# Kernel tuning notes

Measured on AMD Instinct MI355X. Metric: run time of the kernel, lower is better.

The kernel has to match this reference:

```python
import jax, jax.numpy as jnp
import numpy as np

N = 200000      # nodes
E = 200000      # edges per direction
IN = 256        # in_dim
HID = 256       # hidden_dim
HEADS = 4
C = HID // HEADS  # 64 per-head channels
OUT = 128
EPS = 1e-5      # LayerNorm eps (torch default)


def _ln(x, g, b):
    m = jnp.mean(x, axis=-1, keepdims=True)
    v = jnp.mean(jnp.square(x - m), axis=-1, keepdims=True)
    return (x - m) / jnp.sqrt(v + EPS) * g + b


def _gat(x, W, att_src, att_dst, bias, edge_index):
    """PyG GATConv (default args: add_self_loops=True, negative_slope=0.2, concat heads)."""
    n = x.shape[0]
    loops = jnp.arange(n, dtype=edge_index.dtype)
    ei = jnp.concatenate([edge_index, jnp.stack([loops, loops])], axis=1)
    src, dst = ei[0], ei[1]
    h = (x @ W).reshape(n, HEADS, C)                      # [N,H,C]
    a_src = jnp.sum(h * att_src, axis=-1)                 # [N,H]
    a_dst = jnp.sum(h * att_dst, axis=-1)                 # [N,H]
    e = jax.nn.leaky_relu(a_src[src] + a_dst[dst], 0.2)   # [E+N,H]
    m = jax.ops.segment_max(e, dst, num_segments=n)       # per-dst softmax max
    ex = jnp.exp(e - m[dst])
    denom = jax.ops.segment_sum(ex, dst, num_segments=n)
    alpha = ex / denom[dst]                               # [E+N,H]
    out = jax.ops.segment_sum(h[src] * alpha[..., None], dst, num_segments=n)
    return out.reshape(n, HEADS * C) + bias


def setup_inputs() -> dict:
    key = jax.random.key(0)
    ks = jax.random.split(key, 20)
    w = lambda k, s, sc=0.05: jax.random.normal(k, s, jnp.float32) * sc
    return {
        "x": jax.random.normal(ks[0], (N, IN), jnp.float32),
        "edge_index_bu": jax.random.randint(ks[1], (2, E), 0, N, jnp.int32),
        "edge_index_td": jax.random.randint(ks[2], (2, E), 0, N, jnp.int32),
        "Wp": w(ks[3], (IN, HID)), "bp": jnp.zeros((HID,), jnp.float32),
        "W_bu": w(ks[4], (HID, HID)), "asrc_bu": w(ks[5], (HEADS, C)),
        "adst_bu": w(ks[6], (HEADS, C)), "bias_bu": jnp.zeros((HID,), jnp.float32),
        "W_td": w(ks[7], (HID, HID)), "asrc_td": w(ks[8], (HEADS, C)),
        "adst_td": w(ks[9], (HEADS, C)), "bias_td": jnp.zeros((HID,), jnp.float32),
        "Wf": w(ks[10], (2 * HID, OUT)), "bf": jnp.zeros((OUT,), jnp.float32),
        "g_bu": jnp.ones((HID,), jnp.float32), "b_bu": jnp.zeros((HID,), jnp.float32),
        "g_td": jnp.ones((HID,), jnp.float32), "b_td": jnp.zeros((HID,), jnp.float32),
        "g_out": jnp.ones((OUT,), jnp.float32), "b_out": jnp.zeros((OUT,), jnp.float32),
    }


def reference(x, edge_index_bu, edge_index_td, Wp, bp,
              W_bu, asrc_bu, adst_bu, bias_bu,
              W_td, asrc_td, adst_td, bias_td,
              Wf, bf, g_bu, b_bu, g_td, b_td, g_out, b_out):
    h = jax.nn.relu(x @ Wp + bp)  # dropout is identity in eval
    x_bu = jax.nn.relu(_ln(_gat(h, W_bu, asrc_bu, adst_bu, bias_bu, edge_index_bu), g_bu, b_bu))
    x_td = jax.nn.relu(_ln(_gat(h, W_td, asrc_td, adst_td, bias_td, edge_index_td), g_td, b_td))
    out = jnp.concatenate([x_bu, x_td], axis=-1) @ Wf + bf
    out = _ln(out, g_out, b_out)
    nrm = jnp.sqrt(jnp.sum(jnp.square(out), axis=-1, keepdims=True))
    return out / jnp.maximum(nrm, 1e-12)
```

## Files before the change

### kernel.cpp

```cpp
#include <hip/hip_runtime.h>
#include <hip/hip_bf16.h>
#include <stdint.h>


typedef __attribute__((ext_vector_type(8))) short bf16x8;
typedef __attribute__((ext_vector_type(4))) short bf16x4;
typedef __attribute__((ext_vector_type(4))) float f32x4;

#define HID 256

__device__ __forceinline__ float red16(float v) {
    #pragma unroll
    for (int o = 1; o < 16; o <<= 1) v += __shfl_xor(v, o, 64);
    return v;
}
__device__ __forceinline__ float bf2f(short s) {
    return __uint_as_float(((unsigned)(unsigned short)s) << 16);
}

__device__ __forceinline__ void gload_lds16(const void* g, void* l) {
    __builtin_amdgcn_global_load_lds(
        reinterpret_cast<const __attribute__((address_space(1))) uint32_t*>(
            reinterpret_cast<uintptr_t>(g)),
        reinterpret_cast<__attribute__((address_space(3))) uint32_t*>(
            reinterpret_cast<uintptr_t>(l)),
        16, 0, 0);
}

__global__ __launch_bounds__(256) void transpose_all(
    const float* __restrict__ Wp, const float* __restrict__ Wbu,
    const float* __restrict__ Wtd, const float* __restrict__ Wf,
    __hip_bfloat16* __restrict__ Wpt, __hip_bfloat16* __restrict__ Wcat,
    __hip_bfloat16* __restrict__ Wft) {
    int idx = blockIdx.x * 256 + threadIdx.x;
    if (idx < 65536) {
        int k = idx >> 8, j = idx & 255;
        Wpt[j * 256 + k] = __float2bfloat16(Wp[idx]);
    } else if (idx < 131072) {
        int t = idx - 65536; int k = t >> 8, j = t & 255;
        Wcat[j * 256 + k] = __float2bfloat16(Wbu[t]);
    } else if (idx < 196608) {
        int t = idx - 131072; int k = t >> 8, j = t & 255;
        Wcat[65536 + j * 256 + k] = __float2bfloat16(Wtd[t]);
    } else if (idx < 262144) {
        int t = idx - 196608; int k = t >> 7, j = t & 127;
        Wft[(long)j * 512 + k] = __float2bfloat16(Wf[t]);
    }
}

template<int BN, int MODE, int CVT>
__global__ __launch_bounds__(512) void gemm_tiled(
    const float* __restrict__ Af, const __hip_bfloat16* __restrict__ Ab, int lda,
    const __hip_bfloat16* __restrict__ Bt, int KI,
    const float* __restrict__ bias, int doRelu,
    __hip_bfloat16* __restrict__ outB, int ldcB, int colOff,
    float* __restrict__ outF,
    const float* __restrict__ gw, const float* __restrict__ bw, int N) {

    constexpr int WN = BN / 64;
    constexpr int WM = 8 / WN;
    constexpr int MR = (128 / WM) / 16;

    __shared__ __align__(16) __hip_bfloat16 sA[2][128 * 32];
    __shared__ __align__(16) __hip_bfloat16 sB[2][BN * 32];
    __shared__ float sRed[MODE == 2 ? 128 * 4 : 4];
    __shared__ float sN2[MODE == 2 ? 128 * 2 : 2];

    int tid = threadIdx.x;
    int wv = tid >> 6, ln = tid & 63;
    int m = ln & 15, q = ln >> 4;
    long row0 = (long)blockIdx.x * 128;
    int wr = (wv / WN) * (128 / WM);
    int wc = (wv % WN) * 64;

    f32x4 acc[MR][4];
    #pragma unroll
    for (int mi = 0; mi < MR; ++mi)
        #pragma unroll
        for (int t = 0; t < 4; ++t) acc[mi][t] = (f32x4){0.f, 0.f, 0.f, 0.f};

    int oA = tid * 16;
    long rowA = row0 + (oA >> 6);
    if (rowA >= N) rowA = N - 1;
    int kel = (oA & 63) >> 1;
    long aBase = rowA * (long)lda + kel;

    auto stage = [&](int buf, int k0) {
        if constexpr (CVT) {
            const float* src = Af + aBase + k0;
            f32x4 fa0 = *(const f32x4*)src;
            f32x4 fa1 = *(const f32x4*)(src + 4);
            __hip_bfloat16 t8[8];
            t8[0] = __float2bfloat16(fa0[0]); t8[1] = __float2bfloat16(fa0[1]);
            t8[2] = __float2bfloat16(fa0[2]); t8[3] = __float2bfloat16(fa0[3]);
            t8[4] = __float2bfloat16(fa1[0]); t8[5] = __float2bfloat16(fa1[1]);
            t8[6] = __float2bfloat16(fa1[2]); t8[7] = __float2bfloat16(fa1[3]);
            *(bf16x8*)((char*)sA[buf] + oA) = *(const bf16x8*)t8;
        } else {
            gload_lds16(Ab + aBase + k0, (char*)sA[buf] + oA);
        }
        #pragma unroll
        for (int j = 0; j < BN / 128; ++j) {
            int o = j * 8192 + tid * 16;
            const __hip_bfloat16* src = Bt + (long)(o >> 6) * KI + k0 + ((o & 63) >> 1);
            gload_lds16(src, (char*)sB[buf] + o);
        }
    };

    auto compute = [&](int buf) {
        bf16x8 af[MR], bfr[4];
        #pragma unroll
        for (int mi = 0; mi < MR; ++mi)
            af[mi] = *(const bf16x8*)((const char*)sA[buf] + ((wr + mi * 16 + m) << 6) + q * 16);
        #pragma unroll
        for (int t = 0; t < 4; ++t)
            bfr[t] = *(const bf16x8*)((const char*)sB[buf] + ((wc + t * 16 + m) << 6) + q * 16);
        #pragma unroll
        for (int mi = 0; mi < MR; ++mi)
            #pragma unroll
            for (int t = 0; t < 4; ++t)
                acc[mi][t] = __builtin_amdgcn_mfma_f32_16x16x32_bf16(af[mi], bfr[t],
                                                                     acc[mi][t], 0, 0, 0);
    };

    stage(0, 0);
    __syncthreads();
    int cur = 0;
    for (int k0 = 0; k0 < KI; k0 += 32) {
        if (k0 + 32 < KI) stage(cur ^ 1, k0 + 32);
        compute(cur);
        __syncthreads();
        cur ^= 1;
    }

    if constexpr (MODE != 2) {
        #pragma unroll
        for (int mi = 0; mi < MR; ++mi) {
            #pragma unroll
            for (int t = 0; t < 4; ++t) {
                int col = wc + t * 16 + m;
                float bv = bias ? bias[col] : 0.f;
                #pragma unroll
                for (int r = 0; r < 4; ++r) {
                    long row = row0 + wr + mi * 16 + q * 4 + r;
                    if (row < N) {
                        float v = acc[mi][t][r] + bv;
                        if (doRelu) v = fmaxf(v, 0.f);
                        outB[row * ldcB + colOff + col] = __float2bfloat16(v);
                    }
                }
            }
        }
    }

    if constexpr (MODE == 2) {
        float vv[MR][4][4];
        float gcol[4], bcol[4];
        #pragma unroll
        for (int t = 0; t < 4; ++t) {
            int col = wc + t * 16 + m;
            float bb = bias[col];
            gcol[t] = gw[col]; bcol[t] = bw[col];
            #pragma unroll
            for (int mi = 0; mi < MR; ++mi)
                #pragma unroll
                for (int r = 0; r < 4; ++r) vv[mi][t][r] = acc[mi][t][r] + bb;
        }
        int wcid = wc >> 6;
        __syncthreads();
        #pragma unroll
        for (int mi = 0; mi < MR; ++mi) {
            #pragma unroll
            for (int r = 0; r < 4; ++r) {
                float s1 = vv[mi][0][r] + vv[mi][1][r] + vv[mi][2][r] + vv[mi][3][r];
                float s2 = vv[mi][0][r] * vv[mi][0][r] + vv[mi][1][r] * vv[mi][1][r]
                         + vv[mi][2][r] * vv[mi][2][r] + vv[mi][3][r] * vv[mi][3][r];
                s1 = red16(s1); s2 = red16(s2);
                if (m == 0) {
                    int lrow = wr + mi * 16 + q * 4 + r;
                    sRed[lrow * 4 + wcid * 2 + 0] = s1;
                    sRed[lrow * 4 + wcid * 2 + 1] = s2;
                }
            }
        }
        __syncthreads();
        #pragma unroll
        for (int mi = 0; mi < MR; ++mi) {
            #pragma unroll
            for (int r = 0; r < 4; ++r) {
                int lrow = wr + mi * 16 + q * 4 + r;
                float S1 = sRed[lrow * 4 + 0] + sRed[lrow * 4 + 2];
                float S2 = sRed[lrow * 4 + 1] + sRed[lrow * 4 + 3];
                float mean = S1 * (1.f / 128.f);
                float var = S2 * (1.f / 128.f) - mean * mean;
                float inv = rsqrtf(fmaxf(var, 0.f) + 1e-5f);
                float n2 = 0.f;
                #pragma unroll
                for (int t = 0; t < 4; ++t) {
                    float y = (vv[mi][t][r] - mean) * inv * gcol[t] + bcol[t];
                    vv[mi][t][r] = y;
                    n2 += y * y;
                }
                n2 = red16(n2);
                if (m == 0) sN2[lrow * 2 + wcid] = n2;
            }
        }
        __syncthreads();
        #pragma unroll
        for (int mi = 0; mi < MR; ++mi) {
            #pragma unroll
            for (int r = 0; r < 4; ++r) {
                int lrow = wr + mi * 16 + q * 4 + r;
                long row = row0 + lrow;
                float nrm = sqrtf(sN2[lrow * 2] + sN2[lrow * 2 + 1]);
                float sc = 1.f / fmaxf(nrm, 1e-12f);
                if (row < N) {
                    #pragma unroll
                    for (int t = 0; t < 4; ++t)
                        outF[row * 128 + wc + t * 16 + m] = vv[mi][t][r] * sc;
                }
            }
        }
    }
}

__global__ __launch_bounds__(1024) void gemm_dir2(
    const __hip_bfloat16* __restrict__ Ab,
    const __hip_bfloat16* __restrict__ Bt,
    const float* __restrict__ asrc0, const float* __restrict__ adst0,
    const float* __restrict__ asrc1, const float* __restrict__ adst1,
    float* __restrict__ aS0, float* __restrict__ aD0,
    float* __restrict__ aS1, float* __restrict__ aD1,
    __hip_bfloat16* __restrict__ outB, int N) {
    constexpr int KI = 256;
    __shared__ __align__(16) __hip_bfloat16 sA[2][128 * 32];
    __shared__ __align__(16) __hip_bfloat16 sB[2][512 * 32];

    int tid = threadIdx.x;
    int wv = tid >> 6, ln = tid & 63;
    int m = ln & 15, q = ln >> 4;
    long row0 = (long)blockIdx.x * 128;
    int wr = (wv >> 3) * 64;
    int wc = (wv & 7) * 64;

    f32x4 acc[4][4];
    #pragma unroll
    for (int mi = 0; mi < 4; ++mi)
        #pragma unroll
        for (int t = 0; t < 4; ++t) acc[mi][t] = (f32x4){0.f, 0.f, 0.f, 0.f};

    int oA = (tid & 511) * 16;
    long rowA = row0 + (oA >> 6);
    if (rowA >= N) rowA = N - 1;
    int kel = (oA & 63) >> 1;
    long aBase = rowA * (long)KI + kel;
    int oB0 = tid * 16;

    auto stage = [&](int buf, int k0) {
        if (tid < 512) gload_lds16(Ab + aBase + k0, (char*)sA[buf] + oA);
        #pragma unroll
        for (int j = 0; j < 2; ++j) {
            int o = j * 16384 + oB0;
            const __hip_bfloat16* src = Bt + (long)(o >> 6) * KI + k0 + ((o & 63) >> 1);
            gload_lds16(src, (char*)sB[buf] + o);
        }
    };
    auto compute = [&](int buf) {
        bf16x8 af[4], bfr[4];
        #pragma unroll
        for (int mi = 0; mi < 4; ++mi)
            af[mi] = *(const bf16x8*)((const char*)sA[buf] + ((wr + mi * 16 + m) << 6) + q * 16);
        #pragma unroll
        for (int t = 0; t < 4; ++t)
            bfr[t] = *(const bf16x8*)((const char*)sB[buf] + ((wc + t * 16 + m) << 6) + q * 16);
        #pragma unroll
        for (int mi = 0; mi < 4; ++mi)
            #pragma unroll
            for (int t = 0; t < 4; ++t)
                acc[mi][t] = __builtin_amdgcn_mfma_f32_16x16x32_bf16(af[mi], bfr[t],
                                                                     acc[mi][t], 0, 0, 0);
    };

    stage(0, 0);
    __syncthreads();
    int cur = 0;
    for (int k0 = 0; k0 < KI; k0 += 32) {
        if (k0 + 32 < KI) stage(cur ^ 1, k0 + 32);
        compute(cur);
        __syncthreads();
        cur ^= 1;
    }

    #pragma unroll
    for (int mi = 0; mi < 4; ++mi) {
        #pragma unroll
        for (int t = 0; t < 4; ++t) {
            int col = wc + t * 16 + m;
            #pragma unroll
            for (int r = 0; r < 4; ++r) {
                long row = row0 + wr + mi * 16 + q * 4 + r;
                if (row < N) outB[row * 512 + col] = __float2bfloat16(acc[mi][t][r]);
            }
        }
    }

    int dir = wc >> 8;
    int cc = wc & 255;
    int h = cc >> 6;
    const float* as_ = dir ? asrc1 : asrc0;
    const float* ad_ = dir ? adst1 : adst0;
    float* aS = dir ? aS1 : aS0;
    float* aD = dir ? aD1 : aD0;
    f32x4 sw, dw;
    #pragma unroll
    for (int t = 0; t < 4; ++t) {
        sw[t] = as_[cc + t * 16 + m];
        dw[t] = ad_[cc + t * 16 + m];
    }
    #pragma unroll
    for (int mi = 0; mi < 4; ++mi) {
        #pragma unroll
        for (int r = 0; r < 4; ++r) {
            float ps = acc[mi][0][r] * sw[0] + acc[mi][1][r] * sw[1]
                     + acc[mi][2][r] * sw[2] + acc[mi][3][r] * sw[3];
            float pd = acc[mi][0][r] * dw[0] + acc[mi][1][r] * dw[1]
                     + acc[mi][2][r] * dw[2] + acc[mi][3][r] * dw[3];
            ps = red16(ps); pd = red16(pd);
            long row = row0 + wr + mi * 16 + q * 4 + r;
            if (m == 0 && row < N) {
                aS[row * 4 + h] = ps;
                aD[row * 4 + h] = pd;
            }
        }
    }
}

__global__ __launch_bounds__(256) void hist_dst2(const int* __restrict__ ei0,
                                                 const int* __restrict__ ei1,
                                                 int E, int N, int* __restrict__ cnt) {
    int e = blockIdx.x * 256 + threadIdx.x;
    if (e < E) atomicAdd(&cnt[ei0[E + e]], 1);
    else if (e < 2 * E) atomicAdd(&cnt[ei1[e] + N], 1);
}

__global__ __launch_bounds__(256) void scan1(const int* __restrict__ cnt,
                                             int* __restrict__ offpart,
                                             int* __restrict__ bsum, int n) {
    int t = threadIdx.x, i = blockIdx.x * 256 + t;
    int lane = t & 63, w = t >> 6;
    int v = (i < n) ? cnt[i] : 0;
    int inc = v;
    #pragma unroll
    for (int o = 1; o < 64; o <<= 1) {
        int u = __shfl_up(inc, o, 64);
        if (lane >= o) inc += u;
    }
    __shared__ int wsum[4];
    if (lane == 63) wsum[w] = inc;
    __syncthreads();
    int wadd = 0;
    #pragma unroll
    for (int k = 0; k < 4; ++k) if (k < w) wadd += wsum[k];
    if (i < n) offpart[i] = inc - v + wadd;
    if (t == 255) bsum[blockIdx.x] = inc + wadd;
}

__global__ __launch_bounds__(256) void scan2(const int* __restrict__ bsum,
                                             int* __restrict__ btot, int nb) {
    int t = threadIdx.x, lane = t & 63, w = t >> 6;
    int loc[8]; int s = 0;
    #pragma unroll
    for (int k = 0; k < 8; ++k) {
        int idx = t * 8 + k;
        int v = (idx < nb) ? bsum[idx] : 0;
        loc[k] = s; s += v;
    }
    int inc = s;
    #pragma unroll
    for (int o = 1; o < 64; o <<= 1) {
        int u = __shfl_up(inc, o, 64);
        if (lane >= o) inc += u;
    }
    __shared__ int wsum[4];
    if (lane == 63) wsum[w] = inc;
    __syncthreads();
    int wadd = 0;
    #pragma unroll
    for (int k = 0; k < 4; ++k) if (k < w) wadd += wsum[k];
    int excl = inc - s + wadd;
    #pragma unroll
    for (int k = 0; k < 8; ++k) {
        int idx = t * 8 + k;
        if (idx < nb) btot[idx] = excl + loc[k];
    }
}

__global__ __launch_bounds__(256) void finalize_off(const int* __restrict__ offpart,
                                                    const int* __restrict__ btot,
                                                    int* __restrict__ off, int n, int Etot) {
    int i = blockIdx.x * 256 + threadIdx.x;
    if (i < n) off[i] = offpart[i] + btot[i >> 8];
    if (i == 0) off[n] = Etot;
}

__global__ __launch_bounds__(256) void scatter_src2(const int* __restrict__ ei0,
                                                    const int* __restrict__ ei1,
                                                    int E, int N,
                                                    const int* __restrict__ off,
                                                    int* __restrict__ cur,
                                                    int* __restrict__ esrc) {
    int e = blockIdx.x * 256 + threadIdx.x;
    if (e >= 2 * E) return;
    int d, s;
    if (e < E) { d = ei0[E + e]; s = ei0[e]; }
    else       { d = ei1[e] + N; s = ei1[e - E] + N; }
    int pos = off[d] + atomicAdd(&cur[d], 1);
    esrc[pos] = s;
}

__global__ __launch_bounds__(256) void att_alpha(
    const int* __restrict__ off, const int* __restrict__ esrc,
    const float* __restrict__ a_s, const float* __restrict__ a_d,
    float* __restrict__ alpha_self, float* __restrict__ alpha_e, int N2) {
    int d = blockIdx.x * 256 + threadIdx.x;
    if (d >= N2) return;
    int beg = off[d], end = off[d + 1];
    f32x4 adv = *(const f32x4*)(a_d + 4 * (long)d);
    f32x4 asd = *(const f32x4*)(a_s + 4 * (long)d);
    float es[4], m[4];
    #pragma unroll
    for (int h = 0; h < 4; ++h) {
        float e = asd[h] + adv[h]; e = e > 0.f ? e : 0.2f * e;
        es[h] = e; m[h] = e;
    }
    for (int j = beg; j < end; ++j) {
        int s = esrc[j];
        f32x4 asv = *(const f32x4*)(a_s + 4 * (long)s);
        #pragma unroll
        for (int h = 0; h < 4; ++h) {
            float e = asv[h] + adv[h]; e = e > 0.f ? e : 0.2f * e;
            m[h] = fmaxf(m[h], e);
        }
    }
    float sum[4];
    #pragma unroll
    for (int h = 0; h < 4; ++h) sum[h] = __expf(es[h] - m[h]);
    for (int j = beg; j < end; ++j) {
        int s = esrc[j];
        f32x4 asv = *(const f32x4*)(a_s + 4 * (long)s);
        #pragma unroll
        for (int h = 0; h < 4; ++h) {
            float e = asv[h] + adv[h]; e = e > 0.f ? e : 0.2f * e;
            sum[h] += __expf(e - m[h]);
        }
    }
    float rs[4];
    #pragma unroll
    for (int h = 0; h < 4; ++h) rs[h] = 1.f / sum[h];
    f32x4 sa;
    #pragma unroll
    for (int h = 0; h < 4; ++h) sa[h] = __expf(es[h] - m[h]) * rs[h];
    *(f32x4*)(alpha_self + 4 * (long)d) = sa;
    for (int j = beg; j < end; ++j) {
        int s = esrc[j];
        f32x4 asv = *(const f32x4*)(a_s + 4 * (long)s);
        f32x4 av;
        #pragma unroll
        for (int h = 0; h < 4; ++h) {
            float e = asv[h] + adv[h]; e = e > 0.f ? e : 0.2f * e;
            av[h] = __expf(e - m[h]) * rs[h];
        }
        *(f32x4*)(alpha_e + 4 * (long)j) = av;
    }
}

__global__ __launch_bounds__(256) void gat_gather(
    const int* __restrict__ off, const int* __restrict__ esrc,
    const float* __restrict__ alpha_self, const float* __restrict__ alpha_e,
    const __hip_bfloat16* __restrict__ hw,
    const float* __restrict__ bias0, const float* __restrict__ g0,
    const float* __restrict__ b0,
    const float* __restrict__ bias1, const float* __restrict__ g1,
    const float* __restrict__ b1,
    __hip_bfloat16* __restrict__ out, int N) {
    int tid = threadIdx.x;
    int lane = tid & 63;
    int grp = lane >> 4, li = lane & 15;
    long d = (long)blockIdx.x * 16 + (tid >> 6) * 4 + grp;
    if (d >= 2 * (long)N) return;
    int dir = d >= N;
    long dirN = (long)dir * N;
    long pd = d - dirN;
    int dirOff = dir << 8;
    const float* bias = dir ? bias1 : bias0;
    const float* g = dir ? g1 : g0;
    const float* b = dir ? b1 : b0;
    int beg = off[d], end = off[d + 1];
    int head = li >> 2;
    int c0 = li * 16;

    int j = beg;
    bool has = j < end;
    int sN = 0; float aN = 0.f;
    if (has) { sN = esrc[j]; aN = alpha_e[4 * (long)j + head]; }

    float acc[16];
    {
        float a = alpha_self[4 * d + head];
        const __hip_bfloat16* r = hw + pd * 512 + dirOff + c0;
        bf16x8 h0 = *(const bf16x8*)r;
        bf16x8 h1 = *(const bf16x8*)(r + 8);
        #pragma unroll
        for (int k = 0; k < 8; ++k) {
            acc[k] = a * bf2f(h0[k]);
            acc[8 + k] = a * bf2f(h1[k]);
        }
    }
    while (has) {
        long s = (long)sN - dirN;
        float a = aN;
        const __hip_bfloat16* r = hw + s * 512 + dirOff + c0;
        bf16x8 h0 = *(const bf16x8*)r;
        bf16x8 h1 = *(const bf16x8*)(r + 8);
        ++j; has = j < end;
        if (has) {
            sN = esrc[j];
            aN = alpha_e[4 * (long)j + head];
        }
        #pragma unroll
        for (int k = 0; k < 8; ++k) {
            acc[k] += a * bf2f(h0[k]);
            acc[8 + k] += a * bf2f(h1[k]);
        }
    }
    float s1 = 0.f, s2 = 0.f;
    #pragma unroll
    for (int k = 0; k < 16; k += 4) {
        f32x4 bi = *(const f32x4*)(bias + c0 + k);
        #pragma unroll
        for (int u = 0; u < 4; ++u) {
            float v = acc[k + u] + bi[u];
            acc[k + u] = v;
            s1 += v; s2 += v * v;
        }
    }
    #pragma unroll
    for (int o = 1; o < 16; o <<= 1) {
        s1 += __shfl_xor(s1, o, 64);
        s2 += __shfl_xor(s2, o, 64);
    }
    float mean = s1 * (1.f / 256.f);
    float var = s2 * (1.f / 256.f) - mean * mean;
    float inv = rsqrtf(fmaxf(var, 0.f) + 1e-5f);
    __hip_bfloat16 o16[16];
    #pragma unroll
    for (int k = 0; k < 16; k += 4) {
        f32x4 gv = *(const f32x4*)(g + c0 + k);
        f32x4 bv = *(const f32x4*)(b + c0 + k);
        #pragma unroll
        for (int u = 0; u < 4; ++u) {
            float y = (acc[k + u] - mean) * inv * gv[u] + bv[u];
            o16[k + u] = __float2bfloat16(fmaxf(y, 0.f));
        }
    }
    __hip_bfloat16* orow = out + pd * 512 + dirOff + c0;
    *(bf16x8*)orow = *(const bf16x8*)o16;
    *(bf16x8*)(orow + 8) = *(const bf16x8*)(o16 + 8);
}

extern "C" void kernel_launch(void* const* d_in, const int* in_sizes, int n_in,
                              void* d_out, int out_size, void* d_ws, size_t ws_size,
                              hipStream_t stream) {
    const float* x      = (const float*)d_in[0];
    const int*   ei_bu  = (const int*)d_in[1];
    const int*   ei_td  = (const int*)d_in[2];
    const float* Wp     = (const float*)d_in[3];
    const float* bp     = (const float*)d_in[4];
    const float* W_bu   = (const float*)d_in[5];
    const float* asrc_bu= (const float*)d_in[6];
    const float* adst_bu= (const float*)d_in[7];
    const float* bias_bu= (const float*)d_in[8];
    const float* W_td   = (const float*)d_in[9];
    const float* asrc_td= (const float*)d_in[10];
    const float* adst_td= (const float*)d_in[11];
    const float* bias_td= (const float*)d_in[12];
    const float* Wf     = (const float*)d_in[13];
    const float* bfv    = (const float*)d_in[14];
    const float* g_bu   = (const float*)d_in[15];
    const float* b_bu   = (const float*)d_in[16];
    const float* g_td   = (const float*)d_in[17];
    const float* b_td   = (const float*)d_in[18];
    const float* g_out  = (const float*)d_in[19];
    const float* b_out  = (const float*)d_in[20];

    const int N = in_sizes[0] / HID;
    const int E = in_sizes[1] / 2;
    const int N2 = 2 * N, E2 = 2 * E;

    char* ws = (char*)d_ws;
    size_t off0 = 0;
    auto take = [&](size_t bytes) -> char* {
        char* p = ws + off0;
        off0 += (bytes + 255) & ~(size_t)255;
        return p;
    };
    __hip_bfloat16* h_buf = (__hip_bfloat16*)take((size_t)N * 256 * 2);
    __hip_bfloat16* hwcat = (__hip_bfloat16*)take((size_t)N * 512 * 2);
    __hip_bfloat16* xcat  = (__hip_bfloat16*)take((size_t)N * 512 * 2);
    float* aS    = (float*)take((size_t)N2 * 16);
    float* aD    = (float*)take((size_t)N2 * 16);
    float* alsf  = (float*)take((size_t)N2 * 16);
    float* ale   = (float*)take((size_t)E2 * 16);
    int* cnt     = (int*)take((size_t)N2 * 4);
    int* cur     = (int*)take((size_t)N2 * 4);
    int* offpart = (int*)take((size_t)N2 * 4);
    int* offarr  = (int*)take((size_t)(N2 + 1) * 4);
    int* esrc    = (int*)take((size_t)E2 * 4);
    int* bsum    = (int*)take(2048 * 4);
    int* btot    = (int*)take(2048 * 4);
    __hip_bfloat16* Wpt  = (__hip_bfloat16*)take(256 * 256 * 2);
    __hip_bfloat16* Wcat = (__hip_bfloat16*)take(512 * 256 * 2);
    __hip_bfloat16* Wft  = (__hip_bfloat16*)take(128 * 512 * 2);

    transpose_all<<<1024, 256, 0, stream>>>(Wp, W_bu, W_td, Wf, Wpt, Wcat, Wft);

    int gm = (N + 127) / 128;

    gemm_tiled<256, 0, 1><<<gm, 512, 0, stream>>>(
        x, nullptr, 256, Wpt, 256, bp, 1, h_buf, 256, 0, nullptr,
        nullptr, nullptr, N);

    gemm_dir2<<<gm, 1024, 0, stream>>>(
        h_buf, Wcat, asrc_bu, adst_bu, asrc_td, adst_td,
        aS, aD, aS + (size_t)N * 4, aD + (size_t)N * 4, hwcat, N);

    int egrid2 = (E2 + 255) / 256;
    int ngrid2 = (N2 + 255) / 256;
    hipMemsetAsync(cnt, 0, (size_t)N2 * 8, stream);
    hist_dst2<<<egrid2, 256, 0, stream>>>(ei_bu, ei_td, E, N, cnt);
    scan1<<<ngrid2, 256, 0, stream>>>(cnt, offpart, bsum, N2);
    scan2<<<1, 256, 0, stream>>>(bsum, btot, ngrid2);
    finalize_off<<<ngrid2, 256, 0, stream>>>(offpart, btot, offarr, N2, E2);
    scatter_src2<<<egrid2, 256, 0, stream>>>(ei_bu, ei_td, E, N, offarr, cur, esrc);
    att_alpha<<<ngrid2, 256, 0, stream>>>(offarr, esrc, aS, aD, alsf, ale, N2);
    gat_gather<<<(N2 + 15) / 16, 256, 0, stream>>>(offarr, esrc, alsf, ale, hwcat,
                                                   bias_bu, g_bu, b_bu,
                                                   bias_td, g_td, b_td,
                                                   xcat, N);

    gemm_tiled<128, 2, 0><<<gm, 512, 0, stream>>>(
        nullptr, xcat, 512, Wft, 512, bfv, 0, nullptr, 128, 0, (float*)d_out,
        g_out, b_out, N);
}
```

Measured before the change: 810.8 us.

## Fuse attention softmax into gather, histogram into GEMM, zeroing into transpose

Removes the separate att_alpha kernel and computes the per-destination softmax max, sum and weights inside gat_gather per head, eliminating the alpha_self/alpha_e buffers and their writes and reads. The destination histogram is folded into the first GEMM's blocks, and counter zeroing into the transpose kernel, which removes the memset and hist launches. In exchange each gather thread re-reads the source attention scores three times, and the duplicated work across lanes adds exp computations.

```diff
diff --git a/kernel.cpp b/kernel.cpp
--- a/kernel.cpp
+++ b/kernel.cpp
@@ -17,6 +17,7 @@
 __device__ __forceinline__ float bf2f(short s) {
     return __uint_as_float(((unsigned)(unsigned short)s) << 16);
 }
+__device__ __forceinline__ float lrelu(float e) { return e > 0.f ? e : 0.2f * e; }
 
 __device__ __forceinline__ void gload_lds16(const void* g, void* l) {
     __builtin_amdgcn_global_load_lds(
@@ -31,8 +32,9 @@
     const float* __restrict__ Wp, const float* __restrict__ Wbu,
     const float* __restrict__ Wtd, const float* __restrict__ Wf,
     __hip_bfloat16* __restrict__ Wpt, __hip_bfloat16* __restrict__ Wcat,
-    __hip_bfloat16* __restrict__ Wft) {
+    __hip_bfloat16* __restrict__ Wft, int* __restrict__ zeroPtr, int nZero) {
     int idx = blockIdx.x * 256 + threadIdx.x;
+    if (idx < nZero) zeroPtr[idx] = 0;
     if (idx < 65536) {
         int k = idx >> 8, j = idx & 255;
         Wpt[j * 256 + k] = __float2bfloat16(Wp[idx]);
@@ -55,7 +57,9 @@
     const float* __restrict__ bias, int doRelu,
     __hip_bfloat16* __restrict__ outB, int ldcB, int colOff,
     float* __restrict__ outF,
-    const float* __restrict__ gw, const float* __restrict__ bw, int N) {
+    const float* __restrict__ gw, const float* __restrict__ bw,
+    const int* __restrict__ ei0, const int* __restrict__ ei1, int E,
+    int* __restrict__ cntH, int N) {
 
     constexpr int WN = BN / 64;
     constexpr int WM = 8 / WN;
@@ -67,6 +71,15 @@
     __shared__ float sN2[MODE == 2 ? 128 * 2 : 2];
 
     int tid = threadIdx.x;
+
+    if constexpr (MODE == 0) {
+        if (cntH) {
+            int e = blockIdx.x * 512 + tid;
+            if (e < E) atomicAdd(&cntH[ei0[E + e]], 1);
+            else if (e < 2 * E) atomicAdd(&cntH[ei1[e] + N], 1);
+        }
+    }
+
     int wv = tid >> 6, ln = tid & 63;
     int m = ln & 15, q = ln >> 4;
     long row0 = (long)blockIdx.x * 128;
@@ -335,14 +348,6 @@
     }
 }
 
-__global__ __launch_bounds__(256) void hist_dst2(const int* __restrict__ ei0,
-                                                 const int* __restrict__ ei1,
-                                                 int E, int N, int* __restrict__ cnt) {
-    int e = blockIdx.x * 256 + threadIdx.x;
-    if (e < E) atomicAdd(&cnt[ei0[E + e]], 1);
-    else if (e < 2 * E) atomicAdd(&cnt[ei1[e] + N], 1);
-}
-
 __global__ __launch_bounds__(256) void scan1(const int* __restrict__ cnt,
                                              int* __restrict__ offpart,
                                              int* __restrict__ bsum, int n) {
@@ -418,65 +423,9 @@
     esrc[pos] = s;
 }
 
-__global__ __launch_bounds__(256) void att_alpha(
-    const int* __restrict__ off, const int* __restrict__ esrc,
-    const float* __restrict__ a_s, const float* __restrict__ a_d,
-    float* __restrict__ alpha_self, float* __restrict__ alpha_e, int N2) {
-    int d = blockIdx.x * 256 + threadIdx.x;
-    if (d >= N2) return;
-    int beg = off[d], end = off[d + 1];
-    f32x4 adv = *(const f32x4*)(a_d + 4 * (long)d);
-    f32x4 asd = *(const f32x4*)(a_s + 4 * (long)d);
-    float es[4], m[4];
-    #pragma unroll
-    for (int h = 0; h < 4; ++h) {
-        float e = asd[h] + adv[h]; e = e > 0.f ? e : 0.2f * e;
-        es[h] = e; m[h] = e;
-    }
-    for (int j = beg; j < end; ++j) {
-        int s = esrc[j];
-        f32x4 asv = *(const f32x4*)(a_s + 4 * (long)s);
-        #pragma unroll
-        for (int h = 0; h < 4; ++h) {
-            float e = asv[h] + adv[h]; e = e > 0.f ? e : 0.2f * e;
-            m[h] = fmaxf(m[h], e);
-        }
-    }
-    float sum[4];
-    #pragma unroll
-    for (int h = 0; h < 4; ++h) sum[h] = __expf(es[h] - m[h]);
-    for (int j = beg; j < end; ++j) {
-        int s = esrc[j];
-        f32x4 asv = *(const f32x4*)(a_s + 4 * (long)s);
-        #pragma unroll
-        for (int h = 0; h < 4; ++h) {
-            float e = asv[h] + adv[h]; e = e > 0.f ? e : 0.2f * e;
-            sum[h] += __expf(e - m[h]);
-        }
-    }
-    float rs[4];
-    #pragma unroll
-    for (int h = 0; h < 4; ++h) rs[h] = 1.f / sum[h];
-    f32x4 sa;
-    #pragma unroll
-    for (int h = 0; h < 4; ++h) sa[h] = __expf(es[h] - m[h]) * rs[h];
-    *(f32x4*)(alpha_self + 4 * (long)d) = sa;
-    for (int j = beg; j < end; ++j) {
-        int s = esrc[j];
-        f32x4 asv = *(const f32x4*)(a_s + 4 * (long)s);
-        f32x4 av;
-        #pragma unroll
-        for (int h = 0; h < 4; ++h) {
-            float e = asv[h] + adv[h]; e = e > 0.f ? e : 0.2f * e;
-            av[h] = __expf(e - m[h]) * rs[h];
-        }
-        *(f32x4*)(alpha_e + 4 * (long)j) = av;
-    }
-}
-
 __global__ __launch_bounds__(256) void gat_gather(
     const int* __restrict__ off, const int* __restrict__ esrc,
-    const float* __restrict__ alpha_self, const float* __restrict__ alpha_e,
+    const float* __restrict__ aS, const float* __restrict__ aD,
     const __hip_bfloat16* __restrict__ hw,
     const float* __restrict__ bias0, const float* __restrict__ g0,
     const float* __restrict__ b0,
@@ -499,14 +448,23 @@
     int head = li >> 2;
     int c0 = li * 16;
 
-    int j = beg;
-    bool has = j < end;
-    int sN = 0; float aN = 0.f;
-    if (has) { sN = esrc[j]; aN = alpha_e[4 * (long)j + head]; }
+    float adh = aD[4 * d + head];
+    float es = lrelu(aS[4 * d + head] + adh);
+    float mh = es;
+    for (int j = beg; j < end; ++j) {
+        int sv = esrc[j];
+        mh = fmaxf(mh, lrelu(aS[4 * (long)sv + head] + adh));
+    }
+    float sum = __expf(es - mh);
+    for (int j = beg; j < end; ++j) {
+        int sv = esrc[j];
+        sum += __expf(lrelu(aS[4 * (long)sv + head] + adh) - mh);
+    }
+    float rsh = 1.f / sum;
 
     float acc[16];
     {
-        float a = alpha_self[4 * d + head];
+        float a = __expf(es - mh) * rsh;
         const __hip_bfloat16* r = hw + pd * 512 + dirOff + c0;
         bf16x8 h0 = *(const bf16x8*)r;
         bf16x8 h1 = *(const bf16x8*)(r + 8);
@@ -516,17 +474,12 @@
             acc[8 + k] = a * bf2f(h1[k]);
         }
     }
-    while (has) {
-        long s = (long)sN - dirN;
-        float a = aN;
-        const __hip_bfloat16* r = hw + s * 512 + dirOff + c0;
+    for (int j = beg; j < end; ++j) {
+        int sv = esrc[j];
+        float a = __expf(lrelu(aS[4 * (long)sv + head] + adh) - mh) * rsh;
+        const __hip_bfloat16* r = hw + ((long)sv - dirN) * 512 + dirOff + c0;
         bf16x8 h0 = *(const bf16x8*)r;
         bf16x8 h1 = *(const bf16x8*)(r + 8);
-        ++j; has = j < end;
-        if (has) {
-            sN = esrc[j];
-            aN = alpha_e[4 * (long)j + head];
-        }
         #pragma unroll
         for (int k = 0; k < 8; ++k) {
             acc[k] += a * bf2f(h0[k]);
@@ -609,8 +562,6 @@
     __hip_bfloat16* xcat  = (__hip_bfloat16*)take((size_t)N * 512 * 2);
     float* aS    = (float*)take((size_t)N2 * 16);
     float* aD    = (float*)take((size_t)N2 * 16);
-    float* alsf  = (float*)take((size_t)N2 * 16);
-    float* ale   = (float*)take((size_t)E2 * 16);
     int* cnt     = (int*)take((size_t)N2 * 4);
     int* cur     = (int*)take((size_t)N2 * 4);
     int* offpart = (int*)take((size_t)N2 * 4);
@@ -622,13 +573,16 @@
     __hip_bfloat16* Wcat = (__hip_bfloat16*)take(512 * 256 * 2);
     __hip_bfloat16* Wft  = (__hip_bfloat16*)take(128 * 512 * 2);
 
-    transpose_all<<<1024, 256, 0, stream>>>(Wp, W_bu, W_td, Wf, Wpt, Wcat, Wft);
+    int nZero = N2 * 2;
+    int tgrid = (nZero > 262144 ? nZero : 262144);
+    transpose_all<<<(tgrid + 255) / 256, 256, 0, stream>>>(
+        Wp, W_bu, W_td, Wf, Wpt, Wcat, Wft, cnt, nZero);
 
     int gm = (N + 127) / 128;
 
     gemm_tiled<256, 0, 1><<<gm, 512, 0, stream>>>(
         x, nullptr, 256, Wpt, 256, bp, 1, h_buf, 256, 0, nullptr,
-        nullptr, nullptr, N);
+        nullptr, nullptr, ei_bu, ei_td, E, cnt, N);
 
     gemm_dir2<<<gm, 1024, 0, stream>>>(
         h_buf, Wcat, asrc_bu, adst_bu, asrc_td, adst_td,
@@ -636,19 +590,16 @@
 
     int egrid2 = (E2 + 255) / 256;
     int ngrid2 = (N2 + 255) / 256;
-    hipMemsetAsync(cnt, 0, (size_t)N2 * 8, stream);
-    hist_dst2<<<egrid2, 256, 0, stream>>>(ei_bu, ei_td, E, N, cnt);
     scan1<<<ngrid2, 256, 0, stream>>>(cnt, offpart, bsum, N2);
     scan2<<<1, 256, 0, stream>>>(bsum, btot, ngrid2);
     finalize_off<<<ngrid2, 256, 0, stream>>>(offpart, btot, offarr, N2, E2);
     scatter_src2<<<egrid2, 256, 0, stream>>>(ei_bu, ei_td, E, N, offarr, cur, esrc);
-    att_alpha<<<ngrid2, 256, 0, stream>>>(offarr, esrc, aS, aD, alsf, ale, N2);
-    gat_gather<<<(N2 + 15) / 16, 256, 0, stream>>>(offarr, esrc, alsf, ale, hwcat,
+    gat_gather<<<(N2 + 15) / 16, 256, 0, stream>>>(offarr, esrc, aS, aD, hwcat,
                                                    bias_bu, g_bu, b_bu,
                                                    bias_td, g_td, b_td,
                                                    xcat, N);
 
     gemm_tiled<128, 2, 0><<<gm, 512, 0, stream>>>(
         nullptr, xcat, 512, Wft, 512, bfv, 0, nullptr, 128, 0, (float*)d_out,
-        g_out, b_out, N);
-}
+        g_out, b_out, nullptr, nullptr, 0, nullptr, N);
+}
```

Result: slower. 844.9 us (+4.2%).

## Fuse count zeroing and dst histogram into existing kernels, simplify gather loop

Applied to the files above, without the earlier changes.

Zeroing of the count and cursor arrays moves into the weight-transpose kernel, whose grid grows to cover them. The destination-degree histogram atomics move into the prologue of the first projection GEMM. This removes a memset and a separate histogram launch, along with the dependency gaps between them. The GAT gather loop also drops its manual software prefetch of the next edge's source index and alpha in favour of a plain for loop, which may expose more load latency per edge.

```diff
diff --git a/kernel.cpp b/kernel.cpp
--- a/kernel.cpp
+++ b/kernel.cpp
@@ -31,8 +31,9 @@
     const float* __restrict__ Wp, const float* __restrict__ Wbu,
     const float* __restrict__ Wtd, const float* __restrict__ Wf,
     __hip_bfloat16* __restrict__ Wpt, __hip_bfloat16* __restrict__ Wcat,
-    __hip_bfloat16* __restrict__ Wft) {
+    __hip_bfloat16* __restrict__ Wft, int* __restrict__ zeroPtr, int nZero) {
     int idx = blockIdx.x * 256 + threadIdx.x;
+    if (idx < nZero) zeroPtr[idx] = 0;
     if (idx < 65536) {
         int k = idx >> 8, j = idx & 255;
         Wpt[j * 256 + k] = __float2bfloat16(Wp[idx]);
@@ -55,7 +56,9 @@
     const float* __restrict__ bias, int doRelu,
     __hip_bfloat16* __restrict__ outB, int ldcB, int colOff,
     float* __restrict__ outF,
-    const float* __restrict__ gw, const float* __restrict__ bw, int N) {
+    const float* __restrict__ gw, const float* __restrict__ bw,
+    const int* __restrict__ ei0, const int* __restrict__ ei1, int E,
+    int* __restrict__ cntH, int N) {
 
     constexpr int WN = BN / 64;
     constexpr int WM = 8 / WN;
@@ -67,6 +70,15 @@
     __shared__ float sN2[MODE == 2 ? 128 * 2 : 2];
 
     int tid = threadIdx.x;
+
+    if constexpr (MODE == 0) {
+        if (cntH) {
+            int e = blockIdx.x * 512 + tid;
+            if (e < E) atomicAdd(&cntH[ei0[E + e]], 1);
+            else if (e < 2 * E) atomicAdd(&cntH[ei1[e] + N], 1);
+        }
+    }
+
     int wv = tid >> 6, ln = tid & 63;
     int m = ln & 15, q = ln >> 4;
     long row0 = (long)blockIdx.x * 128;
@@ -333,14 +345,6 @@
             }
         }
     }
-}
-
-__global__ __launch_bounds__(256) void hist_dst2(const int* __restrict__ ei0,
-                                                 const int* __restrict__ ei1,
-                                                 int E, int N, int* __restrict__ cnt) {
-    int e = blockIdx.x * 256 + threadIdx.x;
-    if (e < E) atomicAdd(&cnt[ei0[E + e]], 1);
-    else if (e < 2 * E) atomicAdd(&cnt[ei1[e] + N], 1);
 }
 
 __global__ __launch_bounds__(256) void scan1(const int* __restrict__ cnt,
@@ -498,12 +502,6 @@
     int beg = off[d], end = off[d + 1];
     int head = li >> 2;
     int c0 = li * 16;
-
-    int j = beg;
-    bool has = j < end;
-    int sN = 0; float aN = 0.f;
-    if (has) { sN = esrc[j]; aN = alpha_e[4 * (long)j + head]; }
-
     float acc[16];
     {
         float a = alpha_self[4 * d + head];
@@ -516,17 +514,12 @@
             acc[8 + k] = a * bf2f(h1[k]);
         }
     }
-    while (has) {
-        long s = (long)sN - dirN;
-        float a = aN;
+    for (int j = beg; j < end; ++j) {
+        long s = esrc[j] - dirN;
+        float a = alpha_e[4 * (long)j + head];
         const __hip_bfloat16* r = hw + s * 512 + dirOff + c0;
         bf16x8 h0 = *(const bf16x8*)r;
         bf16x8 h1 = *(const bf16x8*)(r + 8);
-        ++j; has = j < end;
-        if (has) {
-            sN = esrc[j];
-            aN = alpha_e[4 * (long)j + head];
-        }
         #pragma unroll
         for (int k = 0; k < 8; ++k) {
             acc[k] += a * bf2f(h0[k]);
@@ -622,13 +615,16 @@
     __hip_bfloat16* Wcat = (__hip_bfloat16*)take(512 * 256 * 2);
     __hip_bfloat16* Wft  = (__hip_bfloat16*)take(128 * 512 * 2);
 
-    transpose_all<<<1024, 256, 0, stream>>>(Wp, W_bu, W_td, Wf, Wpt, Wcat, Wft);
+    int nZero = N2 * 2;
+    int tgrid = (nZero > 262144 ? nZero : 262144);
+    transpose_all<<<(tgrid + 255) / 256, 256, 0, stream>>>(
+        Wp, W_bu, W_td, Wf, Wpt, Wcat, Wft, cnt, nZero);
 
     int gm = (N + 127) / 128;
 
     gemm_tiled<256, 0, 1><<<gm, 512, 0, stream>>>(
         x, nullptr, 256, Wpt, 256, bp, 1, h_buf, 256, 0, nullptr,
-        nullptr, nullptr, N);
+        nullptr, nullptr, ei_bu, ei_td, E, cnt, N);
 
     gemm_dir2<<<gm, 1024, 0, stream>>>(
         h_buf, Wcat, asrc_bu, adst_bu, asrc_td, adst_td,
@@ -636,8 +632,6 @@
 
     int egrid2 = (E2 + 255) / 256;
     int ngrid2 = (N2 + 255) / 256;
-    hipMemsetAsync(cnt, 0, (size_t)N2 * 8, stream);
-    hist_dst2<<<egrid2, 256, 0, stream>>>(ei_bu, ei_td, E, N, cnt);
     scan1<<<ngrid2, 256, 0, stream>>>(cnt, offpart, bsum, N2);
     scan2<<<1, 256, 0, stream>>>(bsum, btot, ngrid2);
     finalize_off<<<ngrid2, 256, 0, stream>>>(offpart, btot, offarr, N2, E2);
@@ -650,5 +644,5 @@
 
     gemm_tiled<128, 2, 0><<<gm, 512, 0, stream>>>(
         nullptr, xcat, 512, Wft, 512, bfv, 0, nullptr, 128, 0, (float*)d_out,
-        g_out, b_out, N);
-}
+        g_out, b_out, nullptr, nullptr, 0, nullptr, N);
+}
```

Result: no change. 807.2 us, median of 2 (-0.4%).
